# Kernel optimization log

Measured on AMD Instinct MI355X. Metric: run time of the kernel, lower is better.

The kernel has to match this reference:

```python
import jax, jax.numpy as jnp
import numpy as np

NUM_HEADS = 8

def setup_inputs() -> dict:
    key = jax.random.key(0)
    ks = jax.random.split(key, 4)
    A, B, H, QD = 256, 256, 2048, 2048
    xav = (6.0 / (H + H)) ** 0.5  # xavier_uniform bound for square weights
    return {
        "q": jax.random.normal(ks[0], (A, B, H), dtype=jnp.float32),
        "k": jax.random.normal(ks[1], (B, QD), dtype=jnp.float32),
        "Wq": jax.random.uniform(ks[2], (H, H), dtype=jnp.float32, minval=-xav, maxval=xav),
        "bq": jnp.zeros((H,), dtype=jnp.float32),
        "Wk": jax.random.uniform(ks[3], (H, QD), dtype=jnp.float32, minval=-xav, maxval=xav),
        "bk": jnp.zeros((H,), dtype=jnp.float32),
    }


def reference(q, k, Wq, bq, Wk, bk):
    n = NUM_HEADS
    H = Wq.shape[0]
    c = H // n
    fact = (H / n) ** -0.5
    # Linear projections (the dominant GEMMs)
    ql = jnp.einsum('abh,oh->abo', q, Wq) + bq          # [A, B, H]
    kl = jnp.einsum('bd,od->bo', k, Wk) + bk            # [B, H]
    A, B, _ = ql.shape
    # permute(1,2,0) then reshape (scrambling reshape, faithful to torch C-order)
    qp = jnp.transpose(ql, (1, 2, 0))                   # [B, H, A]
    qh = qp.reshape(A, B, n, c)                         # [A, B, n, c]
    # k: permute(1,0) -> [H, B], unsqueeze twice -> [H, B, 1, 1], reshape
    kp = jnp.transpose(kl)[:, :, None, None]            # [H, B, 1, 1]
    kh = kp.reshape(B, n, c, 1, 1)                      # [B(q-axis), n, c, 1, 1]
    # attention map einsum; h=w=1 here
    w = jnp.einsum('bqnc,qnchw->bqnhw', qh * fact, kh)  # [A, B, n, 1, 1]
    # softmax over flattened (n*h*w) dims
    w = jax.nn.softmax(w.reshape(A, B, -1), axis=-1).reshape(w.shape)
    return w
```

## Files before the change

kernel.cpp:

```cpp
#include <hip/hip_runtime.h>
#include <stdint.h>


typedef __attribute__((ext_vector_type(8))) __bf16 bf16x8;
typedef __attribute__((ext_vector_type(4))) __bf16 bf16x4;
typedef __attribute__((ext_vector_type(4))) float f32x4;

__device__ __forceinline__ void gload_lds16(const void* g, void* l) {
  __builtin_amdgcn_global_load_lds(
      (const __attribute__((address_space(1))) uint32_t*)g,
      (__attribute__((address_space(3))) uint32_t*)l, 16, 0, 0);
}

__global__ void convert_kernel(const float* __restrict__ qin,
                               const float* __restrict__ Wq,
                               const float* __restrict__ Wk,
                               const float* __restrict__ kin,
                               void* __restrict__ q_t,
                               void* __restrict__ wq_b, void* __restrict__ wk_b,
                               void* __restrict__ k_b) {
  const int NQ0 = 33554432;
  const int NQ1 = 1048576;
  const int NQ2 = 1048576;
  const int NQ3 = 131072;
  const int TOT = NQ0 + NQ1 + NQ2 + NQ3;
  for (int i = blockIdx.x * blockDim.x + threadIdx.x; i < TOT;
       i += gridDim.x * blockDim.x) {
    if (i < NQ0) {
      float4 v = ((const float4*)qin)[i];
      const int jq = i & 511;
      const int b  = (i >> 9) & 255;
      const int c  = i >> 17;
      bf16x4 o;
      o[0] = (__bf16)v.x; o[1] = (__bf16)v.y; o[2] = (__bf16)v.z; o[3] = (__bf16)v.w;
      ((bf16x4*)q_t)[(int64_t)(((b << 8) + c) << 9) + jq] = o;
    } else {
      const float4* src; bf16x4* dst; int j;
      if (i < NQ0+NQ1)              { src = (const float4*)Wq;  dst = (bf16x4*)wq_b; j = i - NQ0; }
      else if (i < NQ0+NQ1+NQ2)     { src = (const float4*)Wk;  dst = (bf16x4*)wk_b; j = i - NQ0 - NQ1; }
      else                          { src = (const float4*)kin; dst = (bf16x4*)k_b;  j = i - NQ0 - NQ1 - NQ2; }
      float4 v = src[j];
      bf16x4 o;
      o[0] = (__bf16)v.x; o[1] = (__bf16)v.y; o[2] = (__bf16)v.z; o[3] = (__bf16)v.w;
      dst[j] = o;
    }
  }
}

__global__ __launch_bounds__(256)
void kl_kernel(const void* __restrict__ k_b, const void* __restrict__ wk_b,
               const float* __restrict__ bk, void* __restrict__ kl_t_v) {
  __shared__ char smem[32768];
  const __bf16* kb   = (const __bf16*)k_b;
  const __bf16* wkb  = (const __bf16*)wk_b;
  __bf16* kl_t = (__bf16*)kl_t_v;
  const int t = threadIdx.x, w = t >> 6, l = t & 63;
  const int ntile = blockIdx.x, mtile = blockIdx.y;
  const int wr = w >> 1, wc = w & 1;
  f32x4 acc[2][2] = {};

  auto stage = [&](int buf, int kt) {
    const int row = t >> 3;
    const int col = (((t & 7) ^ (row & 7)) << 3);
#pragma unroll
    for (int i = 0; i < 2; ++i) {
      const __bf16* ga = kb + (int64_t)(mtile*64 + i*32 + row) * 2048 + kt*64 + col;
      gload_lds16(ga, smem + buf*16384 + (i*256 + w*64)*16);
      const __bf16* gb = wkb + (int64_t)(ntile*64 + i*32 + row) * 2048 + kt*64 + col;
      gload_lds16(gb, smem + buf*16384 + 8192 + (i*256 + w*64)*16);
    }
  };

  stage(0, 0);
  __syncthreads();
  int cur = 0;
  for (int kt = 0; kt < 32; ++kt) {
    if (kt + 1 < 32) stage(cur ^ 1, kt + 1);
    const char* bA = smem + cur*16384;
    const char* bB = smem + cur*16384 + 8192;
#pragma unroll
    for (int kq = 0; kq < 2; ++kq) {
      bf16x8 a[2], b[2];
      const int g = kq*4 + (l >> 4);
#pragma unroll
      for (int mi = 0; mi < 2; ++mi) {
        const int r = wr*32 + mi*16 + (l & 15);
        a[mi] = *(const bf16x8*)(bA + r*128 + ((g ^ (r & 7)) << 4));
      }
#pragma unroll
      for (int ni = 0; ni < 2; ++ni) {
        const int r = wc*32 + ni*16 + (l & 15);
        b[ni] = *(const bf16x8*)(bB + r*128 + ((g ^ (r & 7)) << 4));
      }
#pragma unroll
      for (int mi = 0; mi < 2; ++mi)
#pragma unroll
        for (int ni = 0; ni < 2; ++ni)
          acc[mi][ni] = __builtin_amdgcn_mfma_f32_16x16x32_bf16(a[mi], b[ni], acc[mi][ni], 0, 0, 0);
    }
    __syncthreads();
    cur ^= 1;
  }

#pragma unroll
  for (int ni = 0; ni < 2; ++ni) {
    const int o = ntile*64 + wc*32 + ni*16 + (l & 15);
    const float bko = bk[o];
#pragma unroll
    for (int mi = 0; mi < 2; ++mi) {
      const int c0 = mtile*64 + wr*32 + mi*16 + (l >> 4)*4;
      bf16x4 v;
      v[0] = (__bf16)(acc[mi][ni][0] + bko);
      v[1] = (__bf16)(acc[mi][ni][1] + bko);
      v[2] = (__bf16)(acc[mi][ni][2] + bko);
      v[3] = (__bf16)(acc[mi][ni][3] + bko);
      *(bf16x4*)(kl_t + (int64_t)o*256 + c0) = v;
    }
  }
}

__global__ __launch_bounds__(512, 2)
void main_kernel(const void* __restrict__ q_tv, const void* __restrict__ wq_b,
                 const float* __restrict__ bq, const void* __restrict__ kl_t_v,
                 float* __restrict__ out) {
  __shared__ char smem[163840];
  const __bf16* qt   = (const __bf16*)q_tv;
  const __bf16* wqb  = (const __bf16*)wq_b;
  const __bf16* kl_t = (const __bf16*)kl_t_v;
  const int t = threadIdx.x, w = t >> 6, l = t & 63;
  const int lid = blockIdx.x + 8 * blockIdx.y;
  const int xcd = lid & 7, slot = lid >> 3;
  const int otile = slot & 7;
  const int b = ((slot >> 3) << 3) | xcd;
  const int wr = w >> 2, wc = w & 3;
  f32x4 acc[8][4] = {};

  auto stageA = [&](int buf, int kt, int half) {
#pragma unroll
    for (int i = 0; i < 2; ++i) {
      const int r = i*128 + half*64 + (t >> 3);
      const int sg = (t & 7) ^ (r & 7);
      const __bf16* ga = qt + (int64_t)(b*256 + r) * 2048 + kt*64 + sg*8;
      gload_lds16(ga, smem + buf*32768 + r*128 + (t & 7)*16);
    }
  };
  auto stageB = [&](int buf, int kt, int half) {
#pragma unroll
    for (int i = 0; i < 2; ++i) {
      const int row64 = t >> 3;
      const int r = i*128 + half*32 + (row64 & 31) + ((row64 >> 5) << 6);
      const int sg = (t & 7) ^ (r & 7);
      const __bf16* gb = wqb + (int64_t)(otile*256 + r) * 2048 + kt*64 + sg*8;
      gload_lds16(gb, smem + 98304 + buf*32768 + r*128 + (t & 7)*16);
    }
  };

  auto compute = [&](int abuf, int bbuf) {
    const char* bA_ = smem + abuf*32768;
    const char* bB_ = smem + 98304 + bbuf*32768;
#pragma unroll
    for (int h = 0; h < 2; ++h) {
      const int g_ = h*4 + (l >> 4);
      bf16x8 af[8], bfr[4];
#pragma unroll
      for (int m2 = 0; m2 < 8; ++m2) {
        const int r_ = wr*128 + m2*16 + (l & 15);
        af[m2] = *(const bf16x8*)(bA_ + r_*128 + ((g_ ^ (r_ & 7)) << 4));
      }
#pragma unroll
      for (int n2 = 0; n2 < 4; ++n2) {
        const int r_ = wc*64 + n2*16 + (l & 15);
        bfr[n2] = *(const bf16x8*)(bB_ + r_*128 + ((g_ ^ (r_ & 7)) << 4));
      }
#pragma unroll
      for (int m2 = 0; m2 < 8; ++m2)
#pragma unroll
        for (int n2 = 0; n2 < 4; ++n2)
          acc[m2][n2] = __builtin_amdgcn_mfma_f32_16x16x32_bf16(
              af[m2], bfr[n2], acc[m2][n2], 0, 0, 0);
    }
  };

  stageA(0, 0, 0); stageA(0, 0, 1);
  stageB(0, 0, 0); stageB(0, 0, 1);
  stageA(1, 1, 0); stageA(1, 1, 1);
  asm volatile("s_waitcnt vmcnt(4)" ::: "memory");
  __builtin_amdgcn_s_barrier();

  int ac = 0;
  for (int kt = 0; kt < 32; ++kt) {
    const int as = (ac >= 1) ? ac - 1 : 2;
    const int bc = kt & 1, bs = bc ^ 1;
    if (kt < 31) { stageB(bs, kt + 1, 0); stageB(bs, kt + 1, 1); }
    if (kt < 30) { stageA(as, kt + 2, 0); stageA(as, kt + 2, 1); }
    compute(ac, bc);
    if (kt < 30)      { asm volatile("s_waitcnt vmcnt(4)" ::: "memory"); }
    else if (kt < 31) { asm volatile("s_waitcnt vmcnt(0)" ::: "memory"); }
    __builtin_amdgcn_s_barrier();
    ac = (ac == 2) ? 0 : ac + 1;
  }

  float psum[4] = {0.f, 0.f, 0.f, 0.f};
#pragma unroll
  for (int ni = 0; ni < 4; ++ni) {
    const int o = otile*256 + wc*64 + ni*16 + (l & 15);
    const float bqo = bq[o];
    const __bf16* klc = kl_t + (int64_t)o * 256 + wr*128 + (l >> 4)*4;
#pragma unroll
    for (int mi = 0; mi < 8; ++mi) {
      bf16x4 kv = *(const bf16x4*)(klc + mi*16);
      psum[ni] += (acc[mi][ni][0] + bqo) * (float)kv[0]
                + (acc[mi][ni][1] + bqo) * (float)kv[1]
                + (acc[mi][ni][2] + bqo) * (float)kv[2]
                + (acc[mi][ni][3] + bqo) * (float)kv[3];
    }
  }
#pragma unroll
  for (int ni = 0; ni < 4; ++ni) {
    psum[ni] += __shfl_xor(psum[ni], 16);
    psum[ni] += __shfl_xor(psum[ni], 32);
  }
  float* red = (float*)smem;
  if (l < 16) {
#pragma unroll
    for (int ni = 0; ni < 4; ++ni)
      red[wr*256 + wc*64 + ni*16 + l] = psum[ni];
  }
  __syncthreads();
  if (t < 256) {
    const float s = 0.0625f * (red[t] + red[256 + t]);
    float m = s;
    m = fmaxf(m, __shfl_xor(m, 1));
    m = fmaxf(m, __shfl_xor(m, 2));
    m = fmaxf(m, __shfl_xor(m, 4));
    const float e = __expf(s - m);
    float sum = e;
    sum += __shfl_xor(sum, 1);
    sum += __shfl_xor(sum, 2);
    sum += __shfl_xor(sum, 4);
    out[(int64_t)b*2048 + otile*256 + t] = e / sum;
  }
}

extern "C" void kernel_launch(void* const* d_in, const int* in_sizes, int n_in,
                              void* d_out, int out_size, void* d_ws, size_t ws_size,
                              hipStream_t stream) {
  (void)in_sizes; (void)n_in; (void)out_size; (void)ws_size;
  const float* q  = (const float*)d_in[0];
  const float* k  = (const float*)d_in[1];
  const float* Wq = (const float*)d_in[2];
  const float* bq = (const float*)d_in[3];
  const float* Wk = (const float*)d_in[4];
  const float* bk = (const float*)d_in[5];
  float* out = (float*)d_out;
  char* ws = (char*)d_ws;
  void* q_t  = ws;
  void* wq_b = ws + 268435456;
  void* wk_b = ws + 268435456 + 8388608;
  void* k_b  = ws + 268435456 + 16777216;
  void* kl_t = ws + 268435456 + 17825792;

  convert_kernel<<<2048, 256, 0, stream>>>(q, Wq, Wk, k, q_t, wq_b, wk_b, k_b);
  kl_kernel<<<dim3(32, 4), 256, 0, stream>>>(k_b, wk_b, bk, kl_t);
  main_kernel<<<dim3(8, 256), 512, 0, stream>>>(q_t, wq_b, bq, kl_t, out);
}
```

Measured before the change: 655.7 us.

## Fuse q fp32-to-bf16 conversion into main GEMM register-staged loads

Drops the separate pass that converted and transposed the large q tensor to bf16 in workspace. The main kernel now reads fp32 q directly through registers, converts to bf16 and writes it into swizzled LDS, with a K-tile of 32 and double buffering instead of a triple-buffered A pipeline. This removes a full write and re-read of a 128 MB bf16 copy. In exchange the A loads go through VGPRs, a full vmcnt(0) wait is taken every iteration, and every block (8 per b) now reads fp32 q, double the bytes of the old bf16 copy.

```diff
diff --git a/kernel.cpp b/kernel.cpp
--- a/kernel.cpp
+++ b/kernel.cpp
@@ -12,38 +12,25 @@
       (__attribute__((address_space(3))) uint32_t*)l, 16, 0, 0);
 }
 
-__global__ void convert_kernel(const float* __restrict__ qin,
-                               const float* __restrict__ Wq,
+__global__ void convert_kernel(const float* __restrict__ Wq,
                                const float* __restrict__ Wk,
                                const float* __restrict__ kin,
-                               void* __restrict__ q_t,
                                void* __restrict__ wq_b, void* __restrict__ wk_b,
                                void* __restrict__ k_b) {
-  const int NQ0 = 33554432;
   const int NQ1 = 1048576;
   const int NQ2 = 1048576;
   const int NQ3 = 131072;
-  const int TOT = NQ0 + NQ1 + NQ2 + NQ3;
+  const int TOT = NQ1 + NQ2 + NQ3;
   for (int i = blockIdx.x * blockDim.x + threadIdx.x; i < TOT;
        i += gridDim.x * blockDim.x) {
-    if (i < NQ0) {
-      float4 v = ((const float4*)qin)[i];
-      const int jq = i & 511;
-      const int b  = (i >> 9) & 255;
-      const int c  = i >> 17;
-      bf16x4 o;
-      o[0] = (__bf16)v.x; o[1] = (__bf16)v.y; o[2] = (__bf16)v.z; o[3] = (__bf16)v.w;
-      ((bf16x4*)q_t)[(int64_t)(((b << 8) + c) << 9) + jq] = o;
-    } else {
-      const float4* src; bf16x4* dst; int j;
-      if (i < NQ0+NQ1)              { src = (const float4*)Wq;  dst = (bf16x4*)wq_b; j = i - NQ0; }
-      else if (i < NQ0+NQ1+NQ2)     { src = (const float4*)Wk;  dst = (bf16x4*)wk_b; j = i - NQ0 - NQ1; }
-      else                          { src = (const float4*)kin; dst = (bf16x4*)k_b;  j = i - NQ0 - NQ1 - NQ2; }
-      float4 v = src[j];
-      bf16x4 o;
-      o[0] = (__bf16)v.x; o[1] = (__bf16)v.y; o[2] = (__bf16)v.z; o[3] = (__bf16)v.w;
-      dst[j] = o;
-    }
+    const float4* src; bf16x4* dst; int j;
+    if (i < NQ1)           { src = (const float4*)Wq;  dst = (bf16x4*)wq_b; j = i; }
+    else if (i < NQ1+NQ2)  { src = (const float4*)Wk;  dst = (bf16x4*)wk_b; j = i - NQ1; }
+    else                   { src = (const float4*)kin; dst = (bf16x4*)k_b;  j = i - NQ1 - NQ2; }
+    float4 v = src[j];
+    bf16x4 o;
+    o[0] = (__bf16)v.x; o[1] = (__bf16)v.y; o[2] = (__bf16)v.z; o[3] = (__bf16)v.w;
+    dst[j] = o;
   }
 }
 
@@ -120,11 +107,10 @@
 }
 
 __global__ __launch_bounds__(512, 2)
-void main_kernel(const void* __restrict__ q_tv, const void* __restrict__ wq_b,
+void main_kernel(const float* __restrict__ qf, const void* __restrict__ wq_b,
                  const float* __restrict__ bq, const void* __restrict__ kl_t_v,
                  float* __restrict__ out) {
-  __shared__ char smem[163840];
-  const __bf16* qt   = (const __bf16*)q_tv;
+  __shared__ char smem[65536];
   const __bf16* wqb  = (const __bf16*)wq_b;
   const __bf16* kl_t = (const __bf16*)kl_t_v;
   const int t = threadIdx.x, w = t >> 6, l = t & 63;
@@ -133,71 +119,79 @@
   const int otile = slot & 7;
   const int b = ((slot >> 3) << 3) | xcd;
   const int wr = w >> 2, wc = w & 3;
+  const int crow = t >> 1, chalf = t & 1;
   f32x4 acc[8][4] = {};
 
-  auto stageA = [&](int buf, int kt, int half) {
+  auto loadA = [&](int kt, float4* v) {
+    const float4* src =
+        (const float4*)(qf + (int64_t)(crow*256 + b) * 2048 + kt*32) + chalf*4;
+#pragma unroll
+    for (int j = 0; j < 4; ++j) v[j] = src[j];
+  };
+  auto writeA = [&](int buf, const float4* v) {
+    bf16x8 lo, hi;
+    lo[0]=(__bf16)v[0].x; lo[1]=(__bf16)v[0].y; lo[2]=(__bf16)v[0].z; lo[3]=(__bf16)v[0].w;
+    lo[4]=(__bf16)v[1].x; lo[5]=(__bf16)v[1].y; lo[6]=(__bf16)v[1].z; lo[7]=(__bf16)v[1].w;
+    hi[0]=(__bf16)v[2].x; hi[1]=(__bf16)v[2].y; hi[2]=(__bf16)v[2].z; hi[3]=(__bf16)v[2].w;
+    hi[4]=(__bf16)v[3].x; hi[5]=(__bf16)v[3].y; hi[6]=(__bf16)v[3].z; hi[7]=(__bf16)v[3].w;
+    const int s = crow & 3;
+    char* base = smem + buf*16384 + crow*64;
+    *(bf16x8*)(base + (((2*chalf    ) ^ s) << 4)) = lo;
+    *(bf16x8*)(base + (((2*chalf + 1) ^ s) << 4)) = hi;
+  };
+  auto stageB = [&](int buf, int kt) {
 #pragma unroll
     for (int i = 0; i < 2; ++i) {
-      const int r = i*128 + half*64 + (t >> 3);
-      const int sg = (t & 7) ^ (r & 7);
-      const __bf16* ga = qt + (int64_t)(b*256 + r) * 2048 + kt*64 + sg*8;
-      gload_lds16(ga, smem + buf*32768 + r*128 + (t & 7)*16);
-    }
-  };
-  auto stageB = [&](int buf, int kt, int half) {
-#pragma unroll
-    for (int i = 0; i < 2; ++i) {
-      const int row64 = t >> 3;
-      const int r = i*128 + half*32 + (row64 & 31) + ((row64 >> 5) << 6);
-      const int sg = (t & 7) ^ (r & 7);
-      const __bf16* gb = wqb + (int64_t)(otile*256 + r) * 2048 + kt*64 + sg*8;
-      gload_lds16(gb, smem + 98304 + buf*32768 + r*128 + (t & 7)*16);
-    }
-  };
-
+      const int r = i*128 + (t >> 2);
+      const int sg = (t & 3) ^ (r & 3);
+      const __bf16* gb = wqb + (int64_t)(otile*256 + r) * 2048 + kt*32 + sg*8;
+      gload_lds16(gb, smem + 32768 + buf*16384 + i*8192 + t*16);
+    }
+  };
   auto compute = [&](int abuf, int bbuf) {
-    const char* bA_ = smem + abuf*32768;
-    const char* bB_ = smem + 98304 + bbuf*32768;
-#pragma unroll
-    for (int h = 0; h < 2; ++h) {
-      const int g_ = h*4 + (l >> 4);
-      bf16x8 af[8], bfr[4];
-#pragma unroll
-      for (int m2 = 0; m2 < 8; ++m2) {
-        const int r_ = wr*128 + m2*16 + (l & 15);
-        af[m2] = *(const bf16x8*)(bA_ + r_*128 + ((g_ ^ (r_ & 7)) << 4));
-      }
-#pragma unroll
-      for (int n2 = 0; n2 < 4; ++n2) {
-        const int r_ = wc*64 + n2*16 + (l & 15);
-        bfr[n2] = *(const bf16x8*)(bB_ + r_*128 + ((g_ ^ (r_ & 7)) << 4));
-      }
-#pragma unroll
-      for (int m2 = 0; m2 < 8; ++m2)
-#pragma unroll
-        for (int n2 = 0; n2 < 4; ++n2)
-          acc[m2][n2] = __builtin_amdgcn_mfma_f32_16x16x32_bf16(
-              af[m2], bfr[n2], acc[m2][n2], 0, 0, 0);
-    }
-  };
-
-  stageA(0, 0, 0); stageA(0, 0, 1);
-  stageB(0, 0, 0); stageB(0, 0, 1);
-  stageA(1, 1, 0); stageA(1, 1, 1);
-  asm volatile("s_waitcnt vmcnt(4)" ::: "memory");
+    const char* bA_ = smem + abuf*16384;
+    const char* bB_ = smem + 32768 + bbuf*16384;
+    const int g_ = l >> 4;
+    bf16x8 af[8], bfr[4];
+#pragma unroll
+    for (int m2 = 0; m2 < 8; ++m2) {
+      const int r_ = wr*128 + m2*16 + (l & 15);
+      af[m2] = *(const bf16x8*)(bA_ + r_*64 + ((g_ ^ (r_ & 3)) << 4));
+    }
+#pragma unroll
+    for (int n2 = 0; n2 < 4; ++n2) {
+      const int r_ = wc*64 + n2*16 + (l & 15);
+      bfr[n2] = *(const bf16x8*)(bB_ + r_*64 + ((g_ ^ (r_ & 3)) << 4));
+    }
+#pragma unroll
+    for (int m2 = 0; m2 < 8; ++m2)
+#pragma unroll
+      for (int n2 = 0; n2 < 4; ++n2)
+        acc[m2][n2] = __builtin_amdgcn_mfma_f32_16x16x32_bf16(
+            af[m2], bfr[n2], acc[m2][n2], 0, 0, 0);
+  };
+
+  float4 av[4];
+  loadA(0, av);
+  stageB(0, 0);
+  asm volatile("s_waitcnt vmcnt(0)" ::: "memory");
+  writeA(0, av);
+  asm volatile("s_waitcnt lgkmcnt(0)" ::: "memory");
   __builtin_amdgcn_s_barrier();
 
-  int ac = 0;
-  for (int kt = 0; kt < 32; ++kt) {
-    const int as = (ac >= 1) ? ac - 1 : 2;
-    const int bc = kt & 1, bs = bc ^ 1;
-    if (kt < 31) { stageB(bs, kt + 1, 0); stageB(bs, kt + 1, 1); }
-    if (kt < 30) { stageA(as, kt + 2, 0); stageA(as, kt + 2, 1); }
-    compute(ac, bc);
-    if (kt < 30)      { asm volatile("s_waitcnt vmcnt(4)" ::: "memory"); }
-    else if (kt < 31) { asm volatile("s_waitcnt vmcnt(0)" ::: "memory"); }
+  for (int kt = 0; kt < 64; ++kt) {
+    const int cur = kt & 1, nxt = cur ^ 1;
+    if (kt < 63) {
+      stageB(nxt, kt + 1);
+      loadA(kt + 1, av);
+    }
+    compute(cur, cur);
+    if (kt < 63) {
+      asm volatile("s_waitcnt vmcnt(0)" ::: "memory");
+      writeA(nxt, av);
+    }
+    asm volatile("s_waitcnt lgkmcnt(0)" ::: "memory");
     __builtin_amdgcn_s_barrier();
-    ac = (ac == 2) ? 0 : ac + 1;
   }
 
   float psum[4] = {0.f, 0.f, 0.f, 0.f};
@@ -254,13 +248,12 @@
   const float* bk = (const float*)d_in[5];
   float* out = (float*)d_out;
   char* ws = (char*)d_ws;
-  void* q_t  = ws;
-  void* wq_b = ws + 268435456;
-  void* wk_b = ws + 268435456 + 8388608;
-  void* k_b  = ws + 268435456 + 16777216;
-  void* kl_t = ws + 268435456 + 17825792;
-
-  convert_kernel<<<2048, 256, 0, stream>>>(q, Wq, Wk, k, q_t, wq_b, wk_b, k_b);
+  void* wq_b = ws;
+  void* wk_b = ws + 8388608;
+  void* k_b  = ws + 16777216;
+  void* kl_t = ws + 17825792;
+
+  convert_kernel<<<1024, 256, 0, stream>>>(Wq, Wk, k, wq_b, wk_b, k_b);
   kl_kernel<<<dim3(32, 4), 256, 0, stream>>>(k_b, wk_b, bk, kl_t);
-  main_kernel<<<dim3(8, 256), 512, 0, stream>>>(q_t, wq_b, bq, kl_t, out);
-}
+  main_kernel<<<dim3(8, 256), 512, 0, stream>>>(q, wq_b, bq, kl_t, out);
+}
```

Measured after the change: 1.487 ms. +126.8%, slower.

## Halve GEMM block tile width and K-step to cut LDS and raise occupancy

Applied to the files above, without the earlier changes.

Shrinks the main fused GEMM block from 512 to 256 threads, covering 256x128 outputs instead of 256x256, with a 32-wide K step and a three-stage buffer for both operands. LDS per block drops from 160KB to 72KB, so more blocks can be resident per CU and the grid doubles. In exchange, each q tile is loaded by twice as many blocks, and the loop runs twice as many iterations with barriers and less MFMA work between them.

```diff
diff --git a/kernel.cpp b/kernel.cpp
--- a/kernel.cpp
+++ b/kernel.cpp
@@ -119,91 +119,83 @@
   }
 }
 
-__global__ __launch_bounds__(512, 2)
+__global__ __launch_bounds__(256, 2)
 void main_kernel(const void* __restrict__ q_tv, const void* __restrict__ wq_b,
                  const float* __restrict__ bq, const void* __restrict__ kl_t_v,
                  float* __restrict__ out) {
-  __shared__ char smem[163840];
+  __shared__ char smem[73728];
   const __bf16* qt   = (const __bf16*)q_tv;
   const __bf16* wqb  = (const __bf16*)wq_b;
   const __bf16* kl_t = (const __bf16*)kl_t_v;
   const int t = threadIdx.x, w = t >> 6, l = t & 63;
-  const int lid = blockIdx.x + 8 * blockIdx.y;
+  const int lid = blockIdx.x + 16 * blockIdx.y;
   const int xcd = lid & 7, slot = lid >> 3;
-  const int otile = slot & 7;
-  const int b = ((slot >> 3) << 3) | xcd;
-  const int wr = w >> 2, wc = w & 3;
+  const int otile = slot & 15;
+  const int b = ((slot >> 4) << 3) | xcd;
+  const int wr = w >> 1, wc = w & 1;
   f32x4 acc[8][4] = {};
 
-  auto stageA = [&](int buf, int kt, int half) {
+  auto stageA = [&](int buf, int kt) {
+#pragma unroll
+    for (int i = 0; i < 4; ++i) {
+      const int r = i*64 + (t >> 2);
+      const int sg = (t & 3) ^ (r & 3);
+      const __bf16* ga = qt + (int64_t)(b*256 + r) * 2048 + kt*32 + sg*8;
+      gload_lds16(ga, smem + buf*16384 + r*64 + (t & 3)*16);
+    }
+  };
+  auto stageB = [&](int buf, int kt) {
 #pragma unroll
     for (int i = 0; i < 2; ++i) {
-      const int r = i*128 + half*64 + (t >> 3);
-      const int sg = (t & 7) ^ (r & 7);
-      const __bf16* ga = qt + (int64_t)(b*256 + r) * 2048 + kt*64 + sg*8;
-      gload_lds16(ga, smem + buf*32768 + r*128 + (t & 7)*16);
-    }
-  };
-  auto stageB = [&](int buf, int kt, int half) {
-#pragma unroll
-    for (int i = 0; i < 2; ++i) {
-      const int row64 = t >> 3;
-      const int r = i*128 + half*32 + (row64 & 31) + ((row64 >> 5) << 6);
-      const int sg = (t & 7) ^ (r & 7);
-      const __bf16* gb = wqb + (int64_t)(otile*256 + r) * 2048 + kt*64 + sg*8;
-      gload_lds16(gb, smem + 98304 + buf*32768 + r*128 + (t & 7)*16);
-    }
-  };
-
-  auto compute = [&](int abuf, int bbuf) {
-    const char* bA_ = smem + abuf*32768;
-    const char* bB_ = smem + 98304 + bbuf*32768;
-#pragma unroll
-    for (int h = 0; h < 2; ++h) {
-      const int g_ = h*4 + (l >> 4);
-      bf16x8 af[8], bfr[4];
-#pragma unroll
-      for (int m2 = 0; m2 < 8; ++m2) {
-        const int r_ = wr*128 + m2*16 + (l & 15);
-        af[m2] = *(const bf16x8*)(bA_ + r_*128 + ((g_ ^ (r_ & 7)) << 4));
-      }
-#pragma unroll
-      for (int n2 = 0; n2 < 4; ++n2) {
-        const int r_ = wc*64 + n2*16 + (l & 15);
-        bfr[n2] = *(const bf16x8*)(bB_ + r_*128 + ((g_ ^ (r_ & 7)) << 4));
-      }
-#pragma unroll
-      for (int m2 = 0; m2 < 8; ++m2)
-#pragma unroll
-        for (int n2 = 0; n2 < 4; ++n2)
-          acc[m2][n2] = __builtin_amdgcn_mfma_f32_16x16x32_bf16(
-              af[m2], bfr[n2], acc[m2][n2], 0, 0, 0);
-    }
-  };
-
-  stageA(0, 0, 0); stageA(0, 0, 1);
-  stageB(0, 0, 0); stageB(0, 0, 1);
-  stageA(1, 1, 0); stageA(1, 1, 1);
-  asm volatile("s_waitcnt vmcnt(4)" ::: "memory");
+      const int r = i*64 + (t >> 2);
+      const int sg = (t & 3) ^ (r & 3);
+      const __bf16* gb = wqb + (int64_t)(otile*128 + r) * 2048 + kt*32 + sg*8;
+      gload_lds16(gb, smem + 49152 + buf*8192 + r*64 + (t & 3)*16);
+    }
+  };
+
+  auto compute = [&](int buf) {
+    const char* bA_ = smem + buf*16384;
+    const char* bB_ = smem + 49152 + buf*8192;
+    const int g_ = l >> 4;
+    bf16x8 af[8], bfr[4];
+#pragma unroll
+    for (int m2 = 0; m2 < 8; ++m2) {
+      const int r_ = wr*128 + m2*16 + (l & 15);
+      af[m2] = *(const bf16x8*)(bA_ + r_*64 + ((g_ ^ (r_ & 3)) << 4));
+    }
+#pragma unroll
+    for (int n2 = 0; n2 < 4; ++n2) {
+      const int r_ = wc*64 + n2*16 + (l & 15);
+      bfr[n2] = *(const bf16x8*)(bB_ + r_*64 + ((g_ ^ (r_ & 3)) << 4));
+    }
+#pragma unroll
+    for (int m2 = 0; m2 < 8; ++m2)
+#pragma unroll
+      for (int n2 = 0; n2 < 4; ++n2)
+        acc[m2][n2] = __builtin_amdgcn_mfma_f32_16x16x32_bf16(
+            af[m2], bfr[n2], acc[m2][n2], 0, 0, 0);
+  };
+
+  stageA(0, 0); stageB(0, 0);
+  stageA(1, 1); stageB(1, 1);
+  asm volatile("s_waitcnt vmcnt(6)" ::: "memory");
   __builtin_amdgcn_s_barrier();
 
-  int ac = 0;
-  for (int kt = 0; kt < 32; ++kt) {
-    const int as = (ac >= 1) ? ac - 1 : 2;
-    const int bc = kt & 1, bs = bc ^ 1;
-    if (kt < 31) { stageB(bs, kt + 1, 0); stageB(bs, kt + 1, 1); }
-    if (kt < 30) { stageA(as, kt + 2, 0); stageA(as, kt + 2, 1); }
-    compute(ac, bc);
-    if (kt < 30)      { asm volatile("s_waitcnt vmcnt(4)" ::: "memory"); }
-    else if (kt < 31) { asm volatile("s_waitcnt vmcnt(0)" ::: "memory"); }
+  for (int kt = 0; kt < 64; ++kt) {
+    const int cur = kt % 3;
+    const int nx2 = (kt + 2) % 3;
+    if (kt < 62) { stageA(nx2, kt + 2); stageB(nx2, kt + 2); }
+    compute(cur);
+    if (kt < 62)      { asm volatile("s_waitcnt vmcnt(6)" ::: "memory"); }
+    else if (kt < 63) { asm volatile("s_waitcnt vmcnt(0)" ::: "memory"); }
     __builtin_amdgcn_s_barrier();
-    ac = (ac == 2) ? 0 : ac + 1;
   }
 
   float psum[4] = {0.f, 0.f, 0.f, 0.f};
 #pragma unroll
   for (int ni = 0; ni < 4; ++ni) {
-    const int o = otile*256 + wc*64 + ni*16 + (l & 15);
+    const int o = otile*128 + wc*64 + ni*16 + (l & 15);
     const float bqo = bq[o];
     const __bf16* klc = kl_t + (int64_t)o * 256 + wr*128 + (l >> 4)*4;
 #pragma unroll
@@ -224,11 +216,11 @@
   if (l < 16) {
 #pragma unroll
     for (int ni = 0; ni < 4; ++ni)
-      red[wr*256 + wc*64 + ni*16 + l] = psum[ni];
+      red[wr*128 + wc*64 + ni*16 + l] = psum[ni];
   }
   __syncthreads();
-  if (t < 256) {
-    const float s = 0.0625f * (red[t] + red[256 + t]);
+  if (t < 128) {
+    const float s = 0.0625f * (red[t] + red[128 + t]);
     float m = s;
     m = fmaxf(m, __shfl_xor(m, 1));
     m = fmaxf(m, __shfl_xor(m, 2));
@@ -238,7 +230,7 @@
     sum += __shfl_xor(sum, 1);
     sum += __shfl_xor(sum, 2);
     sum += __shfl_xor(sum, 4);
-    out[(int64_t)b*2048 + otile*256 + t] = e / sum;
+    out[(int64_t)b*2048 + otile*128 + t] = e / sum;
   }
 }
 
@@ -262,5 +254,5 @@
 
   convert_kernel<<<2048, 256, 0, stream>>>(q, Wq, Wk, k, q_t, wq_b, wk_b, k_b);
   kl_kernel<<<dim3(32, 4), 256, 0, stream>>>(k_b, wk_b, bk, kl_t);
-  main_kernel<<<dim3(8, 256), 512, 0, stream>>>(q_t, wq_b, bq, kl_t, out);
-}
+  main_kernel<<<dim3(16, 256), 256, 0, stream>>>(q_t, wq_b, bq, kl_t, out);
+}
```

Measured after the change: 721.5 us. +10.0%, slower.
